# Kernel tuning notes

Measured on AMD Instinct MI355X. Metric: run time of the kernel, lower is better.

The kernel has to match this reference:

```python
import jax, jax.numpy as jnp
import numpy as np

NHEAD = 4

def _layernorm(x, g, b, eps=1e-5):
    m = jnp.mean(x, axis=-1, keepdims=True)
    v = jnp.mean(jnp.square(x - m), axis=-1, keepdims=True)
    return (x - m) * jax.lax.rsqrt(v + eps) * g + b

def setup_inputs() -> dict:
    key = jax.random.key(0)
    ks = jax.random.split(key, 6)
    B, K, L, ninp = 1, 128, 256, 384
    nh, nhid, dim2d, agg_dim = NHEAD, 16, 128, 256
    hc = nh * nhid  # 64
    proj_in = nh * nhid * nhid + dim2d  # 1152
    s = lambda k, shape, sc: (jax.random.normal(k, shape, jnp.float32) * sc)
    return {
        "x1d": s(ks[0], (B, K, L, ninp), 1.0),
        "x2d": s(ks[1], (B, L, L, dim2d), 1.0),
        "Wp": s(ks[2], (ninp, hc), 0.05), "bp": jnp.zeros((hc,), jnp.float32),
        "gp": jnp.ones((hc,), jnp.float32), "betap": jnp.zeros((hc,), jnp.float32),
        "Wq": s(ks[3], (ninp, hc), 0.05), "bq": jnp.zeros((hc,), jnp.float32),
        "Wo": s(ks[4], (proj_in, agg_dim), 0.02), "bo": jnp.zeros((agg_dim,), jnp.float32),
        "go": jnp.ones((agg_dim,), jnp.float32), "betao": jnp.zeros((agg_dim,), jnp.float32),
    }

def reference(x1d, x2d, Wp, bp, gp, betap, Wq, bq, Wo, bo, go, betao):
    B, K, L, _ = x1d.shape
    nh = NHEAD
    # fc_P = Linear + LayerNorm
    P = _layernorm(x1d @ Wp + bp, gp, betap)          # (B,K,L,hc)
    # fc_Q = Linear, then clamp / stable exp over the K (MSA) axis
    Q = jnp.clip(x1d @ Wq + bq, -20.0, 20.0)
    Q = jnp.exp(Q - jnp.max(Q, axis=1, keepdims=True))  # (B,K,L,hc)
    c = P.shape[-1] // nh                              # nhid
    def to_heads(x):
        # (B,K,L,nh*c) -> (B,nh,K,L*c)
        x = x.reshape(B, K, L, nh, c).transpose(0, 3, 1, 2, 4)
        return x.reshape(B, nh, K, L * c)
    Ph = to_heads(P)
    Qh = to_heads(Q)
    PQ = Ph * Qh                                       # elementwise gating
    X = jnp.einsum('bhkm,bhkn->bhmn', PQ, PQ)          # (B,nh,L*c,L*c)
    Y = jnp.einsum('bhkm,bhkn->bhmn', Qh, Qh) + 1e-6
    x = X / Y
    # (B,nh,L,c,L,c) -> (B,L,L,nh*c*c)
    x = x.reshape(B, nh, L, c, L, c).transpose(0, 2, 4, 1, 3, 5).reshape(B, L, L, nh * c * c)
    agg2d = jnp.concatenate([x, x2d], axis=-1)         # (B,L,L,nh*c*c+dim2d)
    out = jax.nn.relu(_layernorm(agg2d @ Wo + bo, go, betao))
    return out
```

## Files before the change

kernel.cpp:

```cpp
#include <hip/hip_runtime.h>
#include <math.h>

#define KNUM 128
#define LL   256
#define NINP 384
#define HC   64
#define NH   4
#define D2   128
#define AGG  256
#define LHC  (LL*HC)
#define M1   (KNUM*LL)
#define PROJ 1152
#define RSTR 1192
#define NELEM 2097152

typedef unsigned short u16;
typedef short bf16x8 __attribute__((ext_vector_type(8)));
typedef float f32x4 __attribute__((ext_vector_type(4)));
typedef unsigned short ushort8 __attribute__((ext_vector_type(8)));

__device__ __forceinline__ void bsplit(float x, u16 &h, u16 &l) {
    unsigned u = __float_as_uint(x);
    unsigned hb = (u + 0x7FFFu + ((u >> 16) & 1u)) >> 16;
    h = (u16)hb;
    float r = x - __uint_as_float(hb << 16);
    unsigned u2 = __float_as_uint(r);
    l = (u16)((u2 + 0x7FFFu + ((u2 >> 16) & 1u)) >> 16);
}

__global__ __launch_bounds__(256) void k_proj(
    const float* __restrict__ x1d, const float* __restrict__ Wp, const float* __restrict__ bp,
    const float* __restrict__ gp, const float* __restrict__ betap,
    const float* __restrict__ Wq, const float* __restrict__ bq,
    float* __restrict__ P, float* __restrict__ Qpre)
{
    __shared__ float Xs[64][33];
    __shared__ float Ws[32][128];
    __shared__ float Ps[64][65];
    const int t = threadIdx.x;
    const int row0 = blockIdx.x * 64;
    const int tc = t & 15, tr = t >> 4;
    float acc[4][8];
    #pragma unroll
    for (int a = 0; a < 4; a++)
        #pragma unroll
        for (int b = 0; b < 8; b++) acc[a][b] = 0.f;

    for (int k0 = 0; k0 < NINP; k0 += 32) {
        for (int idx = t; idx < 64 * 32; idx += 256) {
            int r = idx >> 5, kk = idx & 31;
            Xs[r][kk] = x1d[(size_t)(row0 + r) * NINP + k0 + kk];
        }
        for (int idx = t; idx < 32 * 128; idx += 256) {
            int kk = idx >> 7, cc = idx & 127;
            Ws[kk][cc] = (cc < 64) ? Wp[(size_t)(k0 + kk) * HC + cc]
                                   : Wq[(size_t)(k0 + kk) * HC + (cc - 64)];
        }
        __syncthreads();
        #pragma unroll 4
        for (int kk = 0; kk < 32; kk++) {
            float a[4];
            #pragma unroll
            for (int ri = 0; ri < 4; ri++) a[ri] = Xs[tr * 4 + ri][kk];
            float b[8];
            float4 b0 = *(const float4*)&Ws[kk][tc * 8];
            float4 b1 = *(const float4*)&Ws[kk][tc * 8 + 4];
            b[0]=b0.x; b[1]=b0.y; b[2]=b0.z; b[3]=b0.w;
            b[4]=b1.x; b[5]=b1.y; b[6]=b1.z; b[7]=b1.w;
            #pragma unroll
            for (int ri = 0; ri < 4; ri++)
                #pragma unroll
                for (int ci = 0; ci < 8; ci++) acc[ri][ci] += a[ri] * b[ci];
        }
        __syncthreads();
    }

    #pragma unroll
    for (int ri = 0; ri < 4; ri++) {
        int rloc = tr * 4 + ri;
        size_t r = (size_t)(row0 + rloc);
        #pragma unroll
        for (int ci = 0; ci < 8; ci++) {
            int col = tc * 8 + ci;
            float v = acc[ri][ci];
            if (col < 64) {
                Ps[rloc][col] = v + bp[col];
            } else {
                int qc = col - 64;
                v += bq[qc];
                v = fminf(fmaxf(v, -20.f), 20.f);
                Qpre[r * HC + qc] = v;
            }
        }
    }
    __syncthreads();

    const int wave = t >> 6, lane = t & 63;
    for (int rr = wave * 16; rr < wave * 16 + 16; rr++) {
        float v = Ps[rr][lane];
        float s = v;
        #pragma unroll
        for (int m = 32; m >= 1; m >>= 1) s += __shfl_xor(s, m, 64);
        float mean = s * (1.f / 64.f);
        float d = v - mean;
        float s2 = d * d;
        #pragma unroll
        for (int m = 32; m >= 1; m >>= 1) s2 += __shfl_xor(s2, m, 64);
        float var = s2 * (1.f / 64.f);
        float o = d * rsqrtf(var + 1e-5f) * gp[lane] + betap[lane];
        P[(size_t)(row0 + rr) * HC + lane] = o;
    }
}

__global__ __launch_bounds__(256) void k_qfin(
    const float* __restrict__ P, const float* __restrict__ Qpre,
    u16* __restrict__ PQhi, u16* __restrict__ PQlo,
    u16* __restrict__ Qhi,  u16* __restrict__ Qlo)
{
    __shared__ float qs[128][66];
    __shared__ float ps[128][66];
    __shared__ float red[4][64];
    const int l = blockIdx.x, t = threadIdx.x;
    const int ch = t & 63, kq = t >> 6;

    float m = -1e30f;
    for (int kk = 0; kk < 32; kk++)
        m = fmaxf(m, Qpre[(size_t)(kq * 32 + kk) * LHC + l * HC + ch]);
    red[kq][ch] = m;
    __syncthreads();
    m = fmaxf(fmaxf(red[0][ch], red[1][ch]), fmaxf(red[2][ch], red[3][ch]));
    for (int kk = 0; kk < 32; kk++) {
        int k = kq * 32 + kk;
        size_t g = (size_t)k * LHC + l * HC + ch;
        float q = __expf(Qpre[g] - m);
        qs[k][ch] = q;
        ps[k][ch] = q * P[g];
    }
    __syncthreads();

    const int ch2 = t >> 2, ks = t & 3;
    size_t base = (size_t)l * 8192 + (size_t)ch2 * 128 + ks * 32;
    for (int k8 = 0; k8 < 4; k8++) {
        ushort8 qh, ql, ph, pl;
        #pragma unroll
        for (int e = 0; e < 8; e++) {
            int k = ks * 32 + k8 * 8 + e;
            u16 hh, ll;
            bsplit(qs[k][ch2], hh, ll); qh[e] = hh; ql[e] = ll;
            bsplit(ps[k][ch2], hh, ll); ph[e] = hh; pl[e] = ll;
        }
        *(ushort8*)&Qhi [base + k8 * 8] = qh;
        *(ushort8*)&Qlo [base + k8 * 8] = ql;
        *(ushort8*)&PQhi[base + k8 * 8] = ph;
        *(ushort8*)&PQlo[base + k8 * 8] = pl;
    }
}

__global__ __launch_bounds__(256) void k_prep(
    const float* __restrict__ Wo, u16* __restrict__ WoThi, u16* __restrict__ WoTlo)
{
    __shared__ float ws[16][260];
    const int t = threadIdx.x, r0 = blockIdx.x * 16;
    for (int rr = 0; rr < 16; rr++)
        ws[rr][t] = Wo[(size_t)(r0 + rr) * AGG + t];
    __syncthreads();
    ushort8 h0, l0, h1, l1;
    #pragma unroll
    for (int e = 0; e < 8; e++) {
        u16 hh, ll;
        bsplit(ws[e][t], hh, ll);     h0[e] = hh; l0[e] = ll;
        bsplit(ws[8 + e][t], hh, ll); h1[e] = hh; l1[e] = ll;
    }
    size_t base = (size_t)t * PROJ + r0;
    *(ushort8*)&WoThi[base]     = h0;
    *(ushort8*)&WoThi[base + 8] = h1;
    *(ushort8*)&WoTlo[base]     = l0;
    *(ushort8*)&WoTlo[base + 8] = l1;
}

__global__ __launch_bounds__(512, 2) void k_agg(
    const u16* __restrict__ PQhi, const u16* __restrict__ PQlo,
    const u16* __restrict__ Qhi,  const u16* __restrict__ Qlo,
    const u16* __restrict__ WoThi, const u16* __restrict__ WoTlo,
    const float* __restrict__ x2d, const float* __restrict__ bo,
    const float* __restrict__ go,  const float* __restrict__ betao,
    float* __restrict__ out)
{
    __shared__ __align__(16) u16 smem[76800];
    u16* xlhi = smem;
    u16* xllo = smem + 32 * RSTR;
    u16* Ajh  = smem;
    u16* Ajl  = smem + 10240;
    u16* Aih  = smem + 20480;
    u16* Ail  = smem + 21760;
    float* redmem = (float*)(smem + 76288);

    const int t = threadIdx.x;
    const int ipair = blockIdx.x >> 4, jg = blockIdx.x & 15;
    const int i0 = ipair * 2, j0 = jg * 16;
    const int w  = t >> 6,  l6 = t & 63;
    const int lc = l6 & 15, lg = l6 >> 4;
    const int wi2 = w >> 2, wjq = w & 3;

    f32x4 acc[2][4][4];
    const f32x4 z4 = {0.f, 0.f, 0.f, 0.f};
    #pragma unroll
    for (int p = 0; p < 2; p++)
        #pragma unroll
        for (int h = 0; h < 4; h++)
            #pragma unroll
            for (int jj = 0; jj < 4; jj++) acc[p][h][jj] = z4;

    #pragma unroll
    for (int p = 0; p < 2; p++) {
        const u16* Sh = p ? Qhi : PQhi;
        const u16* Sl = p ? Qlo : PQlo;
        #pragma unroll
        for (int h = 0; h < 4; h++) {
            for (int kw = 0; kw < 4; kw++) {
                __syncthreads();
                for (int idx = t; idx < 2304; idx += 512) {
                    if (idx < 2048) {
                        int pl = idx >> 10, rem = idx & 1023;
                        int j = rem >> 6, ch = (rem >> 2) & 15, q = rem & 3;
                        ushort8 v = *(const ushort8*)&(pl ? Sl : Sh)
                            [(size_t)(j0 + j) * 8192 + (h * 16 + ch) * 128 + kw * 32 + q * 8];
                        *(ushort8*)&(pl ? Ajl : Ajh)[j * 640 + ch * 40 + q * 8] = v;
                    } else {
                        int idx2 = idx - 2048;
                        int pl = idx2 >> 7, rem = idx2 & 127;
                        int i2 = rem >> 6, ch = (rem >> 2) & 15, q = rem & 3;
                        ushort8 v = *(const ushort8*)&(pl ? Sl : Sh)
                            [(size_t)(i0 + i2) * 8192 + (h * 16 + ch) * 128 + kw * 32 + q * 8];
                        *(ushort8*)&(pl ? Ail : Aih)[i2 * 640 + ch * 40 + q * 8] = v;
                    }
                }
                __syncthreads();
                bf16x8 ah = *(const bf16x8*)&Aih[wi2 * 640 + lc * 40 + lg * 8];
                bf16x8 al = *(const bf16x8*)&Ail[wi2 * 640 + lc * 40 + lg * 8];
                #pragma unroll
                for (int jj = 0; jj < 4; jj++) {
                    int j = wjq * 4 + jj;
                    bf16x8 bh = *(const bf16x8*)&Ajh[j * 640 + lc * 40 + lg * 8];
                    bf16x8 bl = *(const bf16x8*)&Ajl[j * 640 + lc * 40 + lg * 8];
                    f32x4 a = acc[p][h][jj];
                    a = __builtin_amdgcn_mfma_f32_16x16x32_bf16(al, bh, a, 0, 0, 0);
                    a = __builtin_amdgcn_mfma_f32_16x16x32_bf16(ah, bl, a, 0, 0, 0);
                    a = __builtin_amdgcn_mfma_f32_16x16x32_bf16(ah, bh, a, 0, 0, 0);
                    acc[p][h][jj] = a;
                }
            }
        }
    }

    __syncthreads();
    #pragma unroll
    for (int h = 0; h < 4; h++)
        #pragma unroll
        for (int jj = 0; jj < 4; jj++) {
            int row = wi2 * 16 + wjq * 4 + jj;
            #pragma unroll
            for (int rg = 0; rg < 4; rg++) {
                float xv = acc[0][h][jj][rg] / (acc[1][h][jj][rg] + 1e-6f);
                int r = h * 256 + (lg * 4 + rg) * 16 + lc;
                u16 hh, ll;
                bsplit(xv, hh, ll);
                xlhi[row * RSTR + r] = hh;
                xllo[row * RSTR + r] = ll;
            }
        }
    for (int idx = t; idx < 4096; idx += 512) {
        int row = idx >> 7, d = idx & 127;
        float v = x2d[(size_t)((i0 + (row >> 4)) * LL + (j0 + (row & 15))) * D2 + d];
        u16 hh, ll;
        bsplit(v, hh, ll);
        xlhi[row * RSTR + 1024 + d] = hh;
        xllo[row * RSTR + 1024 + d] = ll;
    }
    __syncthreads();

    f32x4 accO[2][2];
    accO[0][0] = z4; accO[0][1] = z4; accO[1][0] = z4; accO[1][1] = z4;
    const int nt0 = w * 2;
    for (int ks = 0; ks < 36; ks++) {
        bf16x8 a0h = *(const bf16x8*)&xlhi[(size_t)lc * RSTR + ks * 32 + lg * 8];
        bf16x8 a0l = *(const bf16x8*)&xllo[(size_t)lc * RSTR + ks * 32 + lg * 8];
        bf16x8 a1h = *(const bf16x8*)&xlhi[(size_t)(16 + lc) * RSTR + ks * 32 + lg * 8];
        bf16x8 a1l = *(const bf16x8*)&xllo[(size_t)(16 + lc) * RSTR + ks * 32 + lg * 8];
        #pragma unroll
        for (int n2 = 0; n2 < 2; n2++) {
            size_t wb = (size_t)((nt0 + n2) * 16 + lc) * PROJ + ks * 32 + lg * 8;
            bf16x8 bh = *(const bf16x8*)&WoThi[wb];
            bf16x8 bl = *(const bf16x8*)&WoTlo[wb];
            f32x4 a = accO[0][n2];
            a = __builtin_amdgcn_mfma_f32_16x16x32_bf16(a0l, bh, a, 0, 0, 0);
            a = __builtin_amdgcn_mfma_f32_16x16x32_bf16(a0h, bl, a, 0, 0, 0);
            a = __builtin_amdgcn_mfma_f32_16x16x32_bf16(a0h, bh, a, 0, 0, 0);
            accO[0][n2] = a;
            f32x4 b = accO[1][n2];
            b = __builtin_amdgcn_mfma_f32_16x16x32_bf16(a1l, bh, b, 0, 0, 0);
            b = __builtin_amdgcn_mfma_f32_16x16x32_bf16(a1h, bl, b, 0, 0, 0);
            b = __builtin_amdgcn_mfma_f32_16x16x32_bf16(a1h, bh, b, 0, 0, 0);
            accO[1][n2] = b;
        }
    }

    __syncthreads();
    float* out_lds = (float*)smem;
    #pragma unroll
    for (int mt = 0; mt < 2; mt++)
        #pragma unroll
        for (int n2 = 0; n2 < 2; n2++)
            #pragma unroll
            for (int rg = 0; rg < 4; rg++)
                out_lds[(mt * 16 + lg * 4 + rg) * 260 + (nt0 + n2) * 16 + lc] = accO[mt][n2][rg];
    __syncthreads();

    const int n = t & 255, half = t >> 8;
    const int lane = t & 63, wv4 = (t >> 6) & 3;
    float bon = bo[n], gn = go[n], bn = betao[n];
    float* red1 = redmem;
    float* red2 = redmem + 128;
    float accR[16];
    #pragma unroll
    for (int pp = 0; pp < 16; pp++) {
        int row = half * 16 + pp;
        float v = out_lds[row * 260 + n] + bon;
        accR[pp] = v;
        float s = v;
        #pragma unroll
        for (int m = 32; m >= 1; m >>= 1) s += __shfl_xor(s, m, 64);
        if (lane == 0) red1[row * 4 + wv4] = s;
    }
    __syncthreads();
    #pragma unroll
    for (int pp = 0; pp < 16; pp++) {
        int row = half * 16 + pp;
        float mean = (red1[row*4] + red1[row*4+1] + red1[row*4+2] + red1[row*4+3]) * (1.f / 256.f);
        float d = accR[pp] - mean;
        accR[pp] = d;
        float s2 = d * d;
        #pragma unroll
        for (int m = 32; m >= 1; m >>= 1) s2 += __shfl_xor(s2, m, 64);
        if (lane == 0) red2[row * 4 + wv4] = s2;
    }
    __syncthreads();
    #pragma unroll
    for (int pp = 0; pp < 16; pp++) {
        int row = half * 16 + pp;
        float var = (red2[row*4] + red2[row*4+1] + red2[row*4+2] + red2[row*4+3]) * (1.f / 256.f);
        float o = accR[pp] * rsqrtf(var + 1e-5f) * gn + bn;
        o = fmaxf(o, 0.f);
        out[((size_t)(i0 + half) * LL + (j0 + pp)) * AGG + n] = o;
    }
}

extern "C" void kernel_launch(void* const* d_in, const int* in_sizes, int n_in,
                              void* d_out, int out_size, void* d_ws, size_t ws_size,
                              hipStream_t stream)
{
    const float* x1d   = (const float*)d_in[0];
    const float* x2d   = (const float*)d_in[1];
    const float* Wp    = (const float*)d_in[2];
    const float* bp    = (const float*)d_in[3];
    const float* gp    = (const float*)d_in[4];
    const float* betap = (const float*)d_in[5];
    const float* Wq    = (const float*)d_in[6];
    const float* bq    = (const float*)d_in[7];
    const float* Wo    = (const float*)d_in[8];
    const float* bo    = (const float*)d_in[9];
    const float* go    = (const float*)d_in[10];
    const float* betao = (const float*)d_in[11];
    float* out = (float*)d_out;

    float* P    = (float*)d_ws;
    float* Qpre = P + NELEM;
    u16* PQhi = (u16*)(Qpre + NELEM);
    u16* PQlo = PQhi + NELEM;
    u16* Qhi  = PQlo + NELEM;
    u16* Qlo  = Qhi  + NELEM;
    u16* WoThi = Qlo + NELEM;
    u16* WoTlo = WoThi + 294912;

    hipLaunchKernelGGL(k_prep, dim3(PROJ / 16), dim3(256), 0, stream, Wo, WoThi, WoTlo);
    hipLaunchKernelGGL(k_proj, dim3(M1 / 64), dim3(256), 0, stream,
                       x1d, Wp, bp, gp, betap, Wq, bq, P, Qpre);
    hipLaunchKernelGGL(k_qfin, dim3(LL), dim3(256), 0, stream,
                       P, Qpre, PQhi, PQlo, Qhi, Qlo);
    hipLaunchKernelGGL(k_agg, dim3((LL / 2) * (LL / 16)), dim3(512), 0, stream,
                       PQhi, PQlo, Qhi, Qlo, WoThi, WoTlo, x2d, bo, go, betao, out);
}
```

Before: 1.081 ms.

## Double-buffer LDS staging in k_agg and prefetch Wo fragments across k-steps

The Gram-matrix phase of k_agg now double-buffers its LDS tiles. Global loads for the next (p,h,kw) stage are issued before the MFMAs on the current buffer and written to the other buffer afterwards, so one barrier per stage replaces two. The LDS padding stride changes from 40 to 34 elements to reduce bank conflicts, and s_setprio brackets the MFMA bursts. The output-projection loop is fully unrolled with Wo fragments software-prefetched one k-step ahead. These hide global-load latency behind MFMA work, at the cost of higher register pressure under the 512x2 launch bounds.

New measurement: 1.335 ms. +23.5%, slower.

```diff
diff --git a/kernel.cpp b/kernel.cpp
--- a/kernel.cpp
+++ b/kernel.cpp
@@ -13,6 +13,12 @@
 #define PROJ 1152
 #define RSTR 1192
 #define NELEM 2097152
+
+#define CSTR 34
+#define JSTR (16*CSTR)
+#define AJL_OFF 8704
+#define AI_OFF  17408
+#define BUFSZ   19584
 
 typedef unsigned short u16;
 typedef short bf16x8 __attribute__((ext_vector_type(8)));
@@ -186,14 +192,10 @@
     const float* __restrict__ go,  const float* __restrict__ betao,
     float* __restrict__ out)
 {
-    __shared__ __align__(16) u16 smem[76800];
-    u16* xlhi = smem;
-    u16* xllo = smem + 32 * RSTR;
-    u16* Ajh  = smem;
-    u16* Ajl  = smem + 10240;
-    u16* Aih  = smem + 20480;
-    u16* Ail  = smem + 21760;
-    float* redmem = (float*)(smem + 76288);
+    __shared__ __align__(16) u16 sm[76800];
+    u16* xlhi = sm;
+    u16* xllo = sm + 32 * RSTR;
+    float* redmem = (float*)(sm + 76288);
 
     const int t = threadIdx.x;
     const int ipair = blockIdx.x >> 4, jg = blockIdx.x & 15;
@@ -202,6 +204,48 @@
     const int lc = l6 & 15, lg = l6 >> 4;
     const int wi2 = w >> 2, wjq = w & 3;
 
+    int s_soff[5], s_loff[5], s_pl[5];
+    bool s_valid[5];
+    #pragma unroll
+    for (int s = 0; s < 5; s++) {
+        int idx = t + s * 512;
+        bool val = idx < 2304;
+        s_valid[s] = val;
+        int so = 0, lo = 0, pl = 0;
+        if (val) {
+            if (idx < 2048) {
+                pl = idx >> 10; int rem = idx & 1023;
+                int j = rem >> 6, ch = (rem >> 2) & 15, q = rem & 3;
+                so = (j0 + j) * 8192 + ch * 128 + q * 8;
+                lo = (pl ? AJL_OFF : 0) + j * JSTR + ch * CSTR + q * 8;
+            } else {
+                int idx2 = idx - 2048;
+                pl = idx2 >> 7; int rem = idx2 & 127;
+                int i2 = rem >> 6, ch = (rem >> 2) & 15, q = rem & 3;
+                so = (i0 + i2) * 8192 + ch * 128 + q * 8;
+                lo = AI_OFF + pl * 1088 + i2 * JSTR + ch * CSTR + q * 8;
+            }
+        }
+        s_soff[s] = so; s_loff[s] = lo; s_pl[s] = pl;
+    }
+
+    ushort8 v[5];
+#define EMIT_LOADS(PH, HH, KWW) do {                                        \
+        const u16* _bh = (PH) ? Qhi : PQhi;                                 \
+        const u16* _bl = (PH) ? Qlo : PQlo;                                 \
+        int _rd = (HH) * 2048 + (KWW) * 32;                                 \
+        _Pragma("unroll")                                                   \
+        for (int s = 0; s < 5; s++) if (s_valid[s]) {                       \
+            const u16* _src = s_pl[s] ? _bl : _bh;                          \
+            v[s] = *(const ushort8*)&_src[(size_t)(s_soff[s] + _rd)];       \
+        }                                                                   \
+    } while (0)
+#define WRITE_STAGE(NO) do {                                                \
+        _Pragma("unroll")                                                   \
+        for (int s = 0; s < 5; s++) if (s_valid[s])                         \
+            *(ushort8*)&sm[(NO) + s_loff[s]] = v[s];                        \
+    } while (0)
+
     f32x4 acc[2][4][4];
     const f32x4 z4 = {0.f, 0.f, 0.f, 0.f};
     #pragma unroll
@@ -211,49 +255,52 @@
             #pragma unroll
             for (int jj = 0; jj < 4; jj++) acc[p][h][jj] = z4;
 
+    EMIT_LOADS(0, 0, 0);
+    WRITE_STAGE(0);
+    __syncthreads();
+
     #pragma unroll
     for (int p = 0; p < 2; p++) {
-        const u16* Sh = p ? Qhi : PQhi;
-        const u16* Sl = p ? Qlo : PQlo;
         #pragma unroll
         for (int h = 0; h < 4; h++) {
+            #pragma unroll
             for (int kw = 0; kw < 4; kw++) {
-                __syncthreads();
-                for (int idx = t; idx < 2304; idx += 512) {
-                    if (idx < 2048) {
-                        int pl = idx >> 10, rem = idx & 1023;
-                        int j = rem >> 6, ch = (rem >> 2) & 15, q = rem & 3;
-                        ushort8 v = *(const ushort8*)&(pl ? Sl : Sh)
-                            [(size_t)(j0 + j) * 8192 + (h * 16 + ch) * 128 + kw * 32 + q * 8];
-                        *(ushort8*)&(pl ? Ajl : Ajh)[j * 640 + ch * 40 + q * 8] = v;
-                    } else {
-                        int idx2 = idx - 2048;
-                        int pl = idx2 >> 7, rem = idx2 & 127;
-                        int i2 = rem >> 6, ch = (rem >> 2) & 15, q = rem & 3;
-                        ushort8 v = *(const ushort8*)&(pl ? Sl : Sh)
-                            [(size_t)(i0 + i2) * 8192 + (h * 16 + ch) * 128 + kw * 32 + q * 8];
-                        *(ushort8*)&(pl ? Ail : Aih)[i2 * 640 + ch * 40 + q * 8] = v;
-                    }
+                const int r = ((p * 4 + h) * 4) + kw;
+                if (r + 1 < 32) {
+                    const int rn = r + 1;
+                    const int pn = rn >> 4, hn = (rn >> 2) & 3, kwn = rn & 3;
+                    EMIT_LOADS(pn, hn, kwn);
                 }
-                __syncthreads();
-                bf16x8 ah = *(const bf16x8*)&Aih[wi2 * 640 + lc * 40 + lg * 8];
-                bf16x8 al = *(const bf16x8*)&Ail[wi2 * 640 + lc * 40 + lg * 8];
+                const int cur = (r & 1) ? BUFSZ : 0;
+                const u16* B = sm + cur;
+                bf16x8 ah = *(const bf16x8*)&B[AI_OFF + wi2 * JSTR + lc * CSTR + lg * 8];
+                bf16x8 al = *(const bf16x8*)&B[AI_OFF + 1088 + wi2 * JSTR + lc * CSTR + lg * 8];
+                bf16x8 bhf[4], blf[4];
                 #pragma unroll
                 for (int jj = 0; jj < 4; jj++) {
                     int j = wjq * 4 + jj;
-                    bf16x8 bh = *(const bf16x8*)&Ajh[j * 640 + lc * 40 + lg * 8];
-                    bf16x8 bl = *(const bf16x8*)&Ajl[j * 640 + lc * 40 + lg * 8];
+                    bhf[jj] = *(const bf16x8*)&B[j * JSTR + lc * CSTR + lg * 8];
+                    blf[jj] = *(const bf16x8*)&B[AJL_OFF + j * JSTR + lc * CSTR + lg * 8];
+                }
+                __builtin_amdgcn_s_setprio(1);
+                #pragma unroll
+                for (int jj = 0; jj < 4; jj++) {
                     f32x4 a = acc[p][h][jj];
-                    a = __builtin_amdgcn_mfma_f32_16x16x32_bf16(al, bh, a, 0, 0, 0);
-                    a = __builtin_amdgcn_mfma_f32_16x16x32_bf16(ah, bl, a, 0, 0, 0);
-                    a = __builtin_amdgcn_mfma_f32_16x16x32_bf16(ah, bh, a, 0, 0, 0);
+                    a = __builtin_amdgcn_mfma_f32_16x16x32_bf16(al, bhf[jj], a, 0, 0, 0);
+                    a = __builtin_amdgcn_mfma_f32_16x16x32_bf16(ah, blf[jj], a, 0, 0, 0);
+                    a = __builtin_amdgcn_mfma_f32_16x16x32_bf16(ah, bhf[jj], a, 0, 0, 0);
                     acc[p][h][jj] = a;
                 }
+                __builtin_amdgcn_s_setprio(0);
+                if (r + 1 < 32) {
+                    const int nxt = ((r + 1) & 1) ? BUFSZ : 0;
+                    WRITE_STAGE(nxt);
+                }
+                __syncthreads();
             }
         }
     }
 
-    __syncthreads();
     #pragma unroll
     for (int h = 0; h < 4; h++)
         #pragma unroll
@@ -269,44 +316,80 @@
                 xllo[row * RSTR + r] = ll;
             }
         }
-    for (int idx = t; idx < 4096; idx += 512) {
-        int row = idx >> 7, d = idx & 127;
-        float v = x2d[(size_t)((i0 + (row >> 4)) * LL + (j0 + (row & 15))) * D2 + d];
-        u16 hh, ll;
-        bsplit(v, hh, ll);
-        xlhi[row * RSTR + 1024 + d] = hh;
-        xllo[row * RSTR + 1024 + d] = ll;
+    #pragma unroll
+    for (int it = 0; it < 8; it++) {
+        int idx = t + it * 512;
+        if (idx < 4096) {
+            int row = idx >> 7, d = idx & 127;
+            float val = x2d[(size_t)((i0 + (row >> 4)) * LL + (j0 + (row & 15))) * D2 + d];
+            u16 hh, ll;
+            bsplit(val, hh, ll);
+            xlhi[row * RSTR + 1024 + d] = hh;
+            xllo[row * RSTR + 1024 + d] = ll;
+        }
     }
     __syncthreads();
 
     f32x4 accO[2][2];
     accO[0][0] = z4; accO[0][1] = z4; accO[1][0] = z4; accO[1][1] = z4;
     const int nt0 = w * 2;
-    for (int ks = 0; ks < 36; ks++) {
-        bf16x8 a0h = *(const bf16x8*)&xlhi[(size_t)lc * RSTR + ks * 32 + lg * 8];
-        bf16x8 a0l = *(const bf16x8*)&xllo[(size_t)lc * RSTR + ks * 32 + lg * 8];
-        bf16x8 a1h = *(const bf16x8*)&xlhi[(size_t)(16 + lc) * RSTR + ks * 32 + lg * 8];
-        bf16x8 a1l = *(const bf16x8*)&xllo[(size_t)(16 + lc) * RSTR + ks * 32 + lg * 8];
-        #pragma unroll
-        for (int n2 = 0; n2 < 2; n2++) {
-            size_t wb = (size_t)((nt0 + n2) * 16 + lc) * PROJ + ks * 32 + lg * 8;
-            bf16x8 bh = *(const bf16x8*)&WoThi[wb];
-            bf16x8 bl = *(const bf16x8*)&WoTlo[wb];
-            f32x4 a = accO[0][n2];
-            a = __builtin_amdgcn_mfma_f32_16x16x32_bf16(a0l, bh, a, 0, 0, 0);
-            a = __builtin_amdgcn_mfma_f32_16x16x32_bf16(a0h, bl, a, 0, 0, 0);
-            a = __builtin_amdgcn_mfma_f32_16x16x32_bf16(a0h, bh, a, 0, 0, 0);
-            accO[0][n2] = a;
-            f32x4 b = accO[1][n2];
-            b = __builtin_amdgcn_mfma_f32_16x16x32_bf16(a1l, bh, b, 0, 0, 0);
-            b = __builtin_amdgcn_mfma_f32_16x16x32_bf16(a1h, bl, b, 0, 0, 0);
-            b = __builtin_amdgcn_mfma_f32_16x16x32_bf16(a1h, bh, b, 0, 0, 0);
-            accO[1][n2] = b;
-        }
-    }
-
-    __syncthreads();
-    float* out_lds = (float*)smem;
+    const size_t wrow0 = (size_t)(nt0 * 16 + lc) * PROJ + lg * 8;
+    const size_t wrow1 = (size_t)((nt0 + 1) * 16 + lc) * PROJ + lg * 8;
+
+    bf16x8 Abh0, Abh1, Abl0, Abl1, Bbh0, Bbh1, Bbl0, Bbl1;
+    Abh0 = *(const bf16x8*)&WoThi[wrow0];
+    Abh1 = *(const bf16x8*)&WoThi[wrow1];
+    Abl0 = *(const bf16x8*)&WoTlo[wrow0];
+    Abl1 = *(const bf16x8*)&WoTlo[wrow1];
+
+#define PHB_STEP(KS, BH0, BH1, BL0, BL1) do {                                        \
+        bf16x8 a0h = *(const bf16x8*)&xlhi[(size_t)lc * RSTR + (KS) * 32 + lg * 8];  \
+        bf16x8 a0l = *(const bf16x8*)&xllo[(size_t)lc * RSTR + (KS) * 32 + lg * 8];  \
+        bf16x8 a1h = *(const bf16x8*)&xlhi[(size_t)(16 + lc) * RSTR + (KS) * 32 + lg * 8]; \
+        bf16x8 a1l = *(const bf16x8*)&xllo[(size_t)(16 + lc) * RSTR + (KS) * 32 + lg * 8]; \
+        __builtin_amdgcn_s_setprio(1);                                               \
+        f32x4 a = accO[0][0];                                                        \
+        a = __builtin_amdgcn_mfma_f32_16x16x32_bf16(a0l, BH0, a, 0, 0, 0);           \
+        a = __builtin_amdgcn_mfma_f32_16x16x32_bf16(a0h, BL0, a, 0, 0, 0);           \
+        a = __builtin_amdgcn_mfma_f32_16x16x32_bf16(a0h, BH0, a, 0, 0, 0);           \
+        accO[0][0] = a;                                                              \
+        a = accO[0][1];                                                              \
+        a = __builtin_amdgcn_mfma_f32_16x16x32_bf16(a0l, BH1, a, 0, 0, 0);           \
+        a = __builtin_amdgcn_mfma_f32_16x16x32_bf16(a0h, BL1, a, 0, 0, 0);           \
+        a = __builtin_amdgcn_mfma_f32_16x16x32_bf16(a0h, BH1, a, 0, 0, 0);           \
+        accO[0][1] = a;                                                              \
+        a = accO[1][0];                                                              \
+        a = __builtin_amdgcn_mfma_f32_16x16x32_bf16(a1l, BH0, a, 0, 0, 0);           \
+        a = __builtin_amdgcn_mfma_f32_16x16x32_bf16(a1h, BL0, a, 0, 0, 0);           \
+        a = __builtin_amdgcn_mfma_f32_16x16x32_bf16(a1h, BH0, a, 0, 0, 0);           \
+        accO[1][0] = a;                                                              \
+        a = accO[1][1];                                                              \
+        a = __builtin_amdgcn_mfma_f32_16x16x32_bf16(a1l, BH1, a, 0, 0, 0);           \
+        a = __builtin_amdgcn_mfma_f32_16x16x32_bf16(a1h, BL1, a, 0, 0, 0);           \
+        a = __builtin_amdgcn_mfma_f32_16x16x32_bf16(a1h, BH1, a, 0, 0, 0);           \
+        accO[1][1] = a;                                                              \
+        __builtin_amdgcn_s_setprio(0);                                               \
+    } while (0)
+
+    #pragma unroll
+    for (int ks2 = 0; ks2 < 18; ks2++) {
+        const int ksA = ks2 * 2, ksB = ksA + 1;
+        Bbh0 = *(const bf16x8*)&WoThi[wrow0 + ksB * 32];
+        Bbh1 = *(const bf16x8*)&WoThi[wrow1 + ksB * 32];
+        Bbl0 = *(const bf16x8*)&WoTlo[wrow0 + ksB * 32];
+        Bbl1 = *(const bf16x8*)&WoTlo[wrow1 + ksB * 32];
+        PHB_STEP(ksA, Abh0, Abh1, Abl0, Abl1);
+        if (ks2 < 17) {
+            Abh0 = *(const bf16x8*)&WoThi[wrow0 + (ksA + 2) * 32];
+            Abh1 = *(const bf16x8*)&WoThi[wrow1 + (ksA + 2) * 32];
+            Abl0 = *(const bf16x8*)&WoTlo[wrow0 + (ksA + 2) * 32];
+            Abl1 = *(const bf16x8*)&WoTlo[wrow1 + (ksA + 2) * 32];
+        }
+        PHB_STEP(ksB, Bbh0, Bbh1, Bbl0, Bbl1);
+    }
+
+    __syncthreads();
+    float* out_lds = (float*)sm;
     #pragma unroll
     for (int mt = 0; mt < 2; mt++)
         #pragma unroll
@@ -325,9 +408,9 @@
     #pragma unroll
     for (int pp = 0; pp < 16; pp++) {
         int row = half * 16 + pp;
-        float v = out_lds[row * 260 + n] + bon;
-        accR[pp] = v;
-        float s = v;
+        float val = out_lds[row * 260 + n] + bon;
+        accR[pp] = val;
+        float s = val;
         #pragma unroll
         for (int m = 32; m >= 1; m >>= 1) s += __shfl_xor(s, m, 64);
         if (lane == 0) red1[row * 4 + wv4] = s;
```
